# Kernel tuning notes

Measured on AMD Instinct MI355X. Metric: run time of the kernel, lower is better.

Reference implementation:

```python
import jax, jax.numpy as jnp
import numpy as np

N = 100000   # nodes
E = 1600000  # edges
D = 128      # in_channels (self and agg)
C = 128      # out_channels


def gcn_conv(x, W, b, src, dst, n):
    """PyG GCNConv: add self-loops, symmetric deg normalization, linear, scatter-add."""
    xw = x @ W  # [n, out]
    loops = jnp.arange(n)
    src2 = jnp.concatenate([src, loops])
    dst2 = jnp.concatenate([dst, loops])
    deg = jax.ops.segment_sum(jnp.ones_like(dst2, dtype=xw.dtype), dst2, num_segments=n)
    dinv = jnp.where(deg > 0, jax.lax.rsqrt(deg), 0.0)
    norm = dinv[src2] * dinv[dst2]  # [E+n]
    msg = xw[src2] * norm[:, None]  # gather + scale
    out = jax.ops.segment_sum(msg, dst2, num_segments=n)  # scatter-add at targets
    return out + b


def setup_inputs() -> dict:
    key = jax.random.key(0)
    ks = jax.random.split(key, 16)

    def w(k, shape):
        fan_in = shape[0]
        return (jax.random.uniform(k, shape, jnp.float32, -1.0, 1.0) / np.sqrt(fan_in)).astype(jnp.float32)

    inp = {
        "x_self": jax.random.normal(ks[0], (N, D), jnp.float32),
        "x_neighbor": jax.random.normal(ks[1], (N, D), jnp.float32),
        "edge_index": jax.random.randint(ks[2], (2, E), 0, N, dtype=jnp.int64),
        # linear_in_self: D -> 2C   (weights stored as [in, out])
        "W_in_self": w(ks[3], (D, 2 * C)),
        "b_in_self": w(ks[4], (2 * C,)),
        # linear_out_self: D + 2C -> C
        "W_out_self": w(ks[5], (D + 2 * C, C)),
        "b_out_self": w(ks[6], (C,)),
        # gcn1: D -> 2C ; gcn2: 2C -> C   (gcn3 unused in forward)
        "Wg1": w(ks[7], (D, 2 * C)),
        "bg1": w(ks[8], (2 * C,)),
        "Wg2": w(ks[9], (2 * C, C)),
        "bg2": w(ks[10], (C,)),
        # linear_out: D + 3C -> C
        "W_out": w(ks[11], (D + 3 * C, C)),
        "b_out": w(ks[12], (C,)),
    }
    return inp


def reference(x_self, x_neighbor, edge_index,
              W_in_self, b_in_self, W_out_self, b_out_self,
              Wg1, bg1, Wg2, bg2, W_out, b_out):
    src, dst = edge_index[0], edge_index[1]
    n = x_self.shape[0]

    # dense self branch
    l1 = jax.nn.relu(x_self @ W_in_self + b_in_self)          # [N, 2C]
    l1 = jnp.concatenate([x_self, l1], axis=1)                 # [N, D+2C]
    l1 = l1 @ W_out_self + b_out_self                          # [N, C]

    # GCN neighbor branch
    g1 = gcn_conv(x_neighbor, Wg1, bg1, src, dst, n)           # [N, 2C]
    g2 = gcn_conv(g1, Wg2, bg2, src, dst, n)                   # [N, C]
    x2 = jnp.concatenate([x_neighbor, g1, g2], axis=1)         # [N, D+3C]
    x2 = x2 @ W_out + b_out                                    # [N, C]

    return (l1, x2)
```

## Files before the change

### kernel.cpp

```cpp
#include <hip/hip_runtime.h>
#include <cstdint>
#include <cstddef>

#define NNODES 100000
#define NEDGES 1600000

typedef float f32x4 __attribute__((ext_vector_type(4)));
typedef unsigned int u32;
typedef _Float16 f16x2 __attribute__((ext_vector_type(2)));
typedef _Float16 f16x4 __attribute__((ext_vector_type(4)));
typedef _Float16 f16x8 __attribute__((ext_vector_type(8)));

__device__ __forceinline__ void gload_lds16(const void* g, void* l) {
  __builtin_amdgcn_global_load_lds((const __attribute__((address_space(1))) u32*)g,
                                   (__attribute__((address_space(3))) u32*)l, 16, 0, 0);
}


__global__ void zero_int_kernel(int* __restrict__ p, int n) {
  int i = blockIdx.x * blockDim.x + threadIdx.x;
  if (i < n) p[i] = 0;
}

__global__ void detect_kernel(const unsigned int* __restrict__ ei, int* __restrict__ flag) {
  unsigned int v = ei[2 * threadIdx.x + 1];
  unsigned long long b = __ballot(v != 0u);
  if (threadIdx.x == 0) *flag = (b == 0ull) ? 1 : 0;
}

__device__ __forceinline__ int edge_val(const void* ei, int is64, long long idx) {
  if (is64) return (int)((const long long*)ei)[idx];
  return ((const int*)ei)[idx];
}


__global__ void hist_kernel(const void* __restrict__ ei, const int* __restrict__ flag,
                            int* __restrict__ counts) {
  const int is64 = *flag;
  for (long long e = (long long)blockIdx.x * blockDim.x + threadIdx.x; e < NEDGES;
       e += (long long)gridDim.x * blockDim.x) {
    int d = edge_val(ei, is64, NEDGES + e);
    atomicAdd(&counts[d], 1);
  }
}

__global__ void dinv_kernel(const int* __restrict__ counts, float* __restrict__ dinv) {
  int i = blockIdx.x * blockDim.x + threadIdx.x;
  if (i < NNODES) dinv[i] = rsqrtf((float)(counts[i] + 1));
}

#define SCAN_B 256
#define SCAN_TILE 1024

__global__ void scan_reduce_kernel(const int* __restrict__ counts, int* __restrict__ bsums) {
  __shared__ int sd[SCAN_B];
  int t = threadIdx.x;
  int base = blockIdx.x * SCAN_TILE + t * 4;
  int s = 0;
#pragma unroll
  for (int i = 0; i < 4; i++) {
    int idx = base + i;
    if (idx < NNODES) s += counts[idx];
  }
  sd[t] = s;
  __syncthreads();
  for (int o = SCAN_B / 2; o > 0; o >>= 1) {
    if (t < o) sd[t] += sd[t + o];
    __syncthreads();
  }
  if (t == 0) bsums[blockIdx.x] = sd[0];
}

__global__ void scan_bsums_kernel(int* __restrict__ bsums, int* __restrict__ offs, int nb) {
  if (threadIdx.x == 0 && blockIdx.x == 0) {
    int run = 0;
    for (int b = 0; b < nb; b++) {
      int v = bsums[b];
      bsums[b] = run;
      run += v;
    }
    offs[NNODES] = run;
  }
}

__global__ void scan_write_kernel(const int* __restrict__ counts, const int* __restrict__ bsums,
                                  int* __restrict__ offs) {
  __shared__ int sd[SCAN_B];
  int t = threadIdx.x;
  int base = blockIdx.x * SCAN_TILE + t * 4;
  int v[4];
  int s = 0;
#pragma unroll
  for (int i = 0; i < 4; i++) {
    int idx = base + i;
    v[i] = (idx < NNODES) ? counts[idx] : 0;
    s += v[i];
  }
  sd[t] = s;
  __syncthreads();
  for (int o = 1; o < SCAN_B; o <<= 1) {
    int x = (t >= o) ? sd[t - o] : 0;
    __syncthreads();
    sd[t] += x;
    __syncthreads();
  }
  int run = sd[t] - s + bsums[blockIdx.x];
#pragma unroll
  for (int i = 0; i < 4; i++) {
    int idx = base + i;
    if (idx < NNODES) {
      offs[idx] = run;
      run += v[i];
    }
  }
}


#define BK_SHIFT 8
#define NBUCK 391
#define BCAP 8192
#define WCAP 12288

__global__ __launch_bounds__(256) void bucket_kernel(
    const void* __restrict__ ei, const int* __restrict__ flag, const int* __restrict__ offs,
    int* __restrict__ fillc, int* __restrict__ gcount,
    unsigned long long* __restrict__ bpairs, int* __restrict__ csr) {
  __shared__ int lcount[NBUCK];
  __shared__ int gbase[NBUCK];
  __shared__ int lcur[NBUCK];
  const int is64 = *flag;
  const int chunk = NEDGES / 256;
  const long long e0 = (long long)blockIdx.x * chunk;
  const long long e1 = e0 + chunk;
  for (int i = threadIdx.x; i < NBUCK; i += 256) {
    lcount[i] = 0;
    lcur[i] = 0;
  }
  __syncthreads();
  for (long long e = e0 + threadIdx.x; e < e1; e += 256) {
    int d = edge_val(ei, is64, NEDGES + e);
    atomicAdd(&lcount[d >> BK_SHIFT], 1);
  }
  __syncthreads();
  for (int i = threadIdx.x; i < NBUCK; i += 256) {
    int c = lcount[i];
    gbase[i] = c ? atomicAdd(&gcount[i], c) : 0;
  }
  __syncthreads();
  for (long long e = e0 + threadIdx.x; e < e1; e += 256) {
    int s = edge_val(ei, is64, e);
    int d = edge_val(ei, is64, NEDGES + e);
    int b = d >> BK_SHIFT;
    int pos = gbase[b] + atomicAdd(&lcur[b], 1);
    if (pos < BCAP) {
      bpairs[(size_t)b * BCAP + pos] =
          ((unsigned long long)(unsigned)d << 32) | (unsigned)s;
    } else {
      int p = offs[d] + atomicAdd(&fillc[d], 1);
      csr[p] = s;
    }
  }
}

__global__ __launch_bounds__(256) void fillwin_kernel(
    const unsigned long long* __restrict__ bpairs, const int* __restrict__ gcount,
    const int* __restrict__ offs, int* __restrict__ fillc, int* __restrict__ csr) {
  __shared__ int win[WCAP];
  __shared__ int nfill[256];
  const int b = blockIdx.x;
  const int nlo = b << BK_SHIFT;
  const int nhi = min(nlo + 256, NNODES);
  const int base = offs[nlo];
  const int W = offs[nhi] - base;
  int cnt = gcount[b];
  if (cnt > BCAP) cnt = BCAP;
  if (W <= WCAP) {
    if ((int)threadIdx.x < nhi - nlo) nfill[threadIdx.x] = fillc[nlo + threadIdx.x];
    for (int i = threadIdx.x; i < W; i += 256) win[i] = csr[base + i];
    __syncthreads();
    for (int i = threadIdx.x; i < cnt; i += 256) {
      unsigned long long v = bpairs[(size_t)b * BCAP + i];
      int d = (int)(v >> 32);
      int s = (int)(v & 0xffffffffull);
      int p = offs[d] - base + atomicAdd(&nfill[d - nlo], 1);
      win[p] = s;
    }
    __syncthreads();
    for (int i = threadIdx.x; i < W; i += 256) csr[base + i] = win[i];
  } else {
    for (int i = threadIdx.x; i < cnt; i += 256) {
      unsigned long long v = bpairs[(size_t)b * BCAP + i];
      int d = (int)(v >> 32);
      int s = (int)(v & 0xffffffffull);
      int p = offs[d] + atomicAdd(&fillc[d], 1);
      csr[p] = s;
    }
  }
}


__global__ void xcvt_kernel(const float* __restrict__ x, f16x4* __restrict__ y, int n4) {
  int i = blockIdx.x * blockDim.x + threadIdx.x;
  if (i >= n4) return;
  float4 v = ((const float4*)x)[i];
  f16x4 h;
  h[0] = (_Float16)v.x;
  h[1] = (_Float16)v.y;
  h[2] = (_Float16)v.z;
  h[3] = (_Float16)v.w;
  y[i] = h;
}


__global__ void prescale16_kernel(const f16x4* __restrict__ x, const float* __restrict__ dinv,
                                  f16x4* __restrict__ y) {
  int i = blockIdx.x * blockDim.x + threadIdx.x;
  if (i >= NNODES * 32) return;
  int row = i >> 5;
  float s = dinv[row];
  f16x4 v = x[i];
  f16x4 h;
  h[0] = (_Float16)((float)v[0] * s);
  h[1] = (_Float16)((float)v[1] * s);
  h[2] = (_Float16)((float)v[2] * s);
  h[3] = (_Float16)((float)v[3] * s);
  y[i] = h;
}


__device__ __forceinline__ float2 f16x2_to_f32(f16x2 h) {
  return make_float2((float)h[0], (float)h[1]);
}

__global__ __launch_bounds__(256) void aggregate_half_kernel(
    const f16x2* __restrict__ in, void* __restrict__ out, int out_half,
    const int* __restrict__ offs, const int* __restrict__ csr, const float* __restrict__ dinv,
    const float* __restrict__ bias) {
  int node = blockIdx.x * 4 + (threadIdx.x >> 6);
  if (node >= NNODES) return;
  int ch = threadIdx.x & 63;
  int beg = offs[node], end = offs[node + 1];

  float2 a0 = f16x2_to_f32(in[(size_t)node * 64 + ch]);
  float2 a1 = make_float2(0.f, 0.f);
  float2 a2 = make_float2(0.f, 0.f);
  float2 a3 = make_float2(0.f, 0.f);

  int p = beg;
  for (; p + 8 <= end; p += 8) {
    int j0 = csr[p + 0], j1 = csr[p + 1], j2 = csr[p + 2], j3 = csr[p + 3];
    int j4 = csr[p + 4], j5 = csr[p + 5], j6 = csr[p + 6], j7 = csr[p + 7];
    f16x2 h0 = in[(size_t)j0 * 64 + ch];
    f16x2 h1 = in[(size_t)j1 * 64 + ch];
    f16x2 h2 = in[(size_t)j2 * 64 + ch];
    f16x2 h3 = in[(size_t)j3 * 64 + ch];
    f16x2 h4 = in[(size_t)j4 * 64 + ch];
    f16x2 h5 = in[(size_t)j5 * 64 + ch];
    f16x2 h6 = in[(size_t)j6 * 64 + ch];
    f16x2 h7 = in[(size_t)j7 * 64 + ch];
    float2 v0 = f16x2_to_f32(h0);
    float2 v1 = f16x2_to_f32(h1);
    float2 v2 = f16x2_to_f32(h2);
    float2 v3 = f16x2_to_f32(h3);
    float2 v4 = f16x2_to_f32(h4);
    float2 v5 = f16x2_to_f32(h5);
    float2 v6 = f16x2_to_f32(h6);
    float2 v7 = f16x2_to_f32(h7);
    a0.x += v0.x; a0.y += v0.y;
    a1.x += v1.x; a1.y += v1.y;
    a2.x += v2.x; a2.y += v2.y;
    a3.x += v3.x; a3.y += v3.y;
    a0.x += v4.x; a0.y += v4.y;
    a1.x += v5.x; a1.y += v5.y;
    a2.x += v6.x; a2.y += v6.y;
    a3.x += v7.x; a3.y += v7.y;
  }
  for (; p + 2 <= end; p += 2) {
    int j0 = csr[p], j1 = csr[p + 1];
    float2 v0 = f16x2_to_f32(in[(size_t)j0 * 64 + ch]);
    float2 v1 = f16x2_to_f32(in[(size_t)j1 * 64 + ch]);
    a0.x += v0.x; a0.y += v0.y;
    a1.x += v1.x; a1.y += v1.y;
  }
  if (p < end) {
    float2 v0 = f16x2_to_f32(in[(size_t)csr[p] * 64 + ch]);
    a0.x += v0.x; a0.y += v0.y;
  }

  float di = dinv[node];
  int c = ch * 2;
  float2 r;
  r.x = di * (a0.x + a1.x + a2.x + a3.x);
  r.y = di * (a0.y + a1.y + a2.y + a3.y);
  if (bias) {
    r.x += bias[c];
    r.y += bias[c + 1];
  }
  if (out_half) {
    f16x2 h;
    h[0] = (_Float16)r.x;
    h[1] = (_Float16)r.y;
    ((f16x2*)out)[(size_t)node * 64 + ch] = h;
  } else {
    *(float2*)((float*)out + (size_t)node * 128 + c) = r;
  }
}


__global__ void wprep_f16_kernel(const float* __restrict__ W, int K, int M,
                                 _Float16* __restrict__ th) {
  int i = blockIdx.x * blockDim.x + threadIdx.x;
  if (i >= K * M) return;
  int k = i / M, m = i - k * M;
  th[(size_t)m * K + k] = (_Float16)W[i];
}


#define BM 128
#define BN 128
#define BK 32

__global__ __launch_bounds__(256) void gemm_f16_kernel(
    const _Float16* __restrict__ A0, int K0, const _Float16* __restrict__ A1, int K1,
    const _Float16* __restrict__ A2, int K2, const _Float16* __restrict__ Bth, int Ktot, int M,
    const float* __restrict__ bias, const float* __restrict__ row_scale,
    void* __restrict__ Cmat, int relu, int out_half, int nrows) {
  __shared__ _Float16 smem[4 * BM * BK];
  _Float16* const As0 = smem;
  _Float16* const Bs0 = smem + 2 * BM * BK;

  const int tid = threadIdx.x;
  const int lane = tid & 63;
  const int wv = tid >> 6;
  const int mBase = (wv >> 1) * 64;
  const int nBase = (wv & 1) * 64;
  const int ml = lane & 15;
  const int quad = lane >> 4;
  const int rowBase = blockIdx.x * BM;
  const int colBase = blockIdx.y * BN;

  const int lrow = lane >> 2;
  const int lslot = lane & 3;

  f32x4 acc[4][4];
  const f32x4 zero = {0.f, 0.f, 0.f, 0.f};
#pragma unroll
  for (int i = 0; i < 4; i++)
#pragma unroll
    for (int j = 0; j < 4; j++) acc[i][j] = zero;

  auto stage = [&](int k0, int buf) {
    const _Float16* Ap;
    int kl, Kp;
    if (k0 < K0) {
      Ap = A0; kl = k0; Kp = K0;
    } else if (k0 < K0 + K1) {
      Ap = A1; kl = k0 - K0; Kp = K1;
    } else {
      Ap = A2; kl = k0 - K0 - K1; Kp = K2;
    }
    char* Ab = (char*)(As0 + buf * BM * BK);
    char* Bb = (char*)(Bs0 + buf * BN * BK);
#pragma unroll
    for (int c = 0; c < 2; c++) {
      int trow = wv * 32 + c * 16 + lrow;
      int sws = lslot ^ (trow & 3);
      size_t ldsoff = (size_t)(wv * 32 + c * 16) * 64;
      int gr = rowBase + trow;
      if (gr > nrows - 1) gr = nrows - 1;
      gload_lds16(Ap + (size_t)gr * Kp + kl + sws * 8, Ab + ldsoff);
      gload_lds16(Bth + (size_t)(colBase + trow) * Ktot + k0 + sws * 8, Bb + ldsoff);
    }
  };

  const int ntile = Ktot / BK;
  stage(0, 0);
  __syncthreads();
  int cur = 0;
  for (int t = 0; t < ntile; ++t) {
    if (t + 1 < ntile) stage((t + 1) * BK, cur ^ 1);

    f16x8 av[4], bv[4];
#pragma unroll
    for (int nt = 0; nt < 4; nt++) {
      int nrow = nBase + nt * 16 + ml;
      int boff = nrow * 32 + ((quad ^ (nrow & 3)) << 3);
      bv[nt] = *(const f16x8*)&Bs0[cur * BN * BK + boff];
    }
#pragma unroll
    for (int mt = 0; mt < 4; mt++) {
      int mrow = mBase + mt * 16 + ml;
      int aoff = mrow * 32 + ((quad ^ (mrow & 3)) << 3);
      av[mt] = *(const f16x8*)&As0[cur * BM * BK + aoff];
    }
#pragma unroll
    for (int mt = 0; mt < 4; mt++)
#pragma unroll
      for (int nt = 0; nt < 4; nt++) {
        acc[mt][nt] =
            __builtin_amdgcn_mfma_f32_16x16x32_f16(av[mt], bv[nt], acc[mt][nt], 0, 0, 0);
      }
    __syncthreads();
    cur ^= 1;
  }

  if (out_half) {
    _Float16* Ct = smem;
#pragma unroll
    for (int nt = 0; nt < 4; nt++) {
      int colL = nBase + nt * 16 + ml;
      float bv = bias ? bias[colBase + colL] : 0.f;
#pragma unroll
      for (int mt = 0; mt < 4; mt++) {
        int rowL0 = mBase + mt * 16 + quad * 4;
#pragma unroll
        for (int r = 0; r < 4; r++) {
          int rowL = rowL0 + r;
          int grow = rowBase + rowL;
          float v = acc[mt][nt][r];
          if (row_scale) v *= row_scale[grow < nrows ? grow : nrows - 1];
          v += bv;
          if (relu) v = fmaxf(v, 0.f);
          Ct[rowL * 128 + colL] = (_Float16)v;
        }
      }
    }
    __syncthreads();
    for (int idx = tid; idx < 2048; idx += 256) {
      int rowL = idx >> 4;
      int chunk = idx & 15;
      int grow = rowBase + rowL;
      if (grow < nrows) {
        *(uint4*)((_Float16*)Cmat + (size_t)grow * M + colBase + chunk * 8) =
            *(const uint4*)&Ct[rowL * 128 + chunk * 8];
      }
    }
  } else {
#pragma unroll
    for (int nt = 0; nt < 4; nt++) {
      int col = colBase + nBase + nt * 16 + ml;
      float bv = bias ? bias[col] : 0.f;
#pragma unroll
      for (int mt = 0; mt < 4; mt++) {
        int row0 = rowBase + mBase + mt * 16 + quad * 4;
#pragma unroll
        for (int r = 0; r < 4; r++) {
          int grow = row0 + r;
          if (grow >= nrows) continue;
          float v = acc[mt][nt][r];
          if (row_scale) v *= row_scale[grow];
          v += bv;
          if (relu) v = fmaxf(v, 0.f);
          ((float*)Cmat)[(size_t)grow * M + col] = v;
        }
      }
    }
  }
}


extern "C" void kernel_launch(void* const* d_in, const int* in_sizes, int n_in, void* d_out,
                              int out_size, void* d_ws, size_t ws_size, hipStream_t stream) {
  const float* x_self     = (const float*)d_in[0];
  const float* x_neighbor = (const float*)d_in[1];
  const void*  edge_index = d_in[2];
  const float* W_in_self  = (const float*)d_in[3];
  const float* b_in_self  = (const float*)d_in[4];
  const float* W_out_self = (const float*)d_in[5];
  const float* b_out_self = (const float*)d_in[6];
  const float* Wg1        = (const float*)d_in[7];
  const float* bg1        = (const float*)d_in[8];
  const float* Wg2        = (const float*)d_in[9];
  const float* bg2        = (const float*)d_in[10];
  const float* W_out      = (const float*)d_in[11];
  const float* b_out      = (const float*)d_in[12];
  float* out = (float*)d_out;

  char* ws = (char*)d_ws;
  size_t off = 0;
  auto alloc = [&](size_t bytes) -> void* {
    void* p = ws + off;
    off = (off + bytes + 255) & ~(size_t)255;
    return p;
  };
  int* counts = (int*)alloc((size_t)2 * NNODES * 4 + 2048);
  int* fillc  = counts + NNODES;
  int* gcount = counts + 2 * NNODES;
  int*   offs   = (int*)alloc((size_t)(NNODES + 1) * 4);
  int*   csr    = (int*)alloc((size_t)NEDGES * 4);
  int*   bsums  = (int*)alloc(4096);
  int*   flag   = (int*)alloc(256);
  float* dinv   = (float*)alloc((size_t)NNODES * 4);
  _Float16* wt1 = (_Float16*)alloc(32768 * 2);
  _Float16* wt2 = (_Float16*)alloc(49152 * 2);
  _Float16* wt3 = (_Float16*)alloc(32768 * 2);
  _Float16* wt4 = (_Float16*)alloc(32768 * 2);
  _Float16* wt5 = (_Float16*)alloc(65536 * 2);
  float* bufA = (float*)alloc((size_t)NNODES * 256 * 4);
  float* bufB = (float*)alloc((size_t)NNODES * 256 * 4);
  (void)ws_size;

  unsigned long long* bpairs = (unsigned long long*)bufA;

  const int nb = (NNODES + SCAN_TILE - 1) / SCAN_TILE;
  const int gridRows = (NNODES + BM - 1) / BM;

  detect_kernel<<<1, 64, 0, stream>>>((const unsigned int*)edge_index, flag);
  zero_int_kernel<<<(2 * NNODES + 512 + 255) / 256, 256, 0, stream>>>(counts,
                                                                      2 * NNODES + 512);
  hist_kernel<<<1024, 256, 0, stream>>>(edge_index, flag, counts);
  dinv_kernel<<<(NNODES + 255) / 256, 256, 0, stream>>>(counts, dinv);
  scan_reduce_kernel<<<nb, SCAN_B, 0, stream>>>(counts, bsums);
  scan_bsums_kernel<<<1, 64, 0, stream>>>(bsums, offs, nb);
  scan_write_kernel<<<nb, SCAN_B, 0, stream>>>(counts, bsums, offs);
  bucket_kernel<<<256, 256, 0, stream>>>(edge_index, flag, offs, fillc, gcount, bpairs, csr);
  fillwin_kernel<<<NBUCK, 256, 0, stream>>>(bpairs, gcount, offs, fillc, csr);

  wprep_f16_kernel<<<(32768 + 255) / 256, 256, 0, stream>>>(W_in_self, 128, 256, wt1);
  wprep_f16_kernel<<<(49152 + 255) / 256, 256, 0, stream>>>(W_out_self, 384, 128, wt2);
  wprep_f16_kernel<<<(32768 + 255) / 256, 256, 0, stream>>>(Wg1, 128, 256, wt3);
  wprep_f16_kernel<<<(32768 + 255) / 256, 256, 0, stream>>>(Wg2, 256, 128, wt4);
  wprep_f16_kernel<<<(65536 + 255) / 256, 256, 0, stream>>>(W_out, 512, 128, wt5);

  _Float16* xs16 = (_Float16*)(bufB + (size_t)NNODES * 128);
  _Float16* xn16 = xs16 + (size_t)NNODES * 128;
  xcvt_kernel<<<(NNODES * 32 + 255) / 256, 256, 0, stream>>>(x_self, (f16x4*)xs16, NNODES * 32);
  xcvt_kernel<<<(NNODES * 32 + 255) / 256, 256, 0, stream>>>(x_neighbor, (f16x4*)xn16,
                                                             NNODES * 32);

  _Float16* l1 = (_Float16*)bufA;
  gemm_f16_kernel<<<dim3(gridRows, 2), 256, 0, stream>>>(
      xs16, 128, nullptr, 0, nullptr, 0, wt1, 128, 256, b_in_self, nullptr, l1, 1, 1, NNODES);
  gemm_f16_kernel<<<dim3(gridRows, 1), 256, 0, stream>>>(
      xs16, 128, l1, 256, nullptr, 0, wt2, 384, 128, b_out_self, nullptr, out, 0, 0, NNODES);

  _Float16* ybuf = (_Float16*)bufB;
  _Float16* aggx = (_Float16*)bufA;
  _Float16* g1   = (_Float16*)bufB;
  _Float16* xw2  = (_Float16*)bufA;
  _Float16* g2   = (_Float16*)bufA + (size_t)NNODES * 128;

  prescale16_kernel<<<(NNODES * 32 + 255) / 256, 256, 0, stream>>>((const f16x4*)xn16, dinv,
                                                                   (f16x4*)ybuf);
  aggregate_half_kernel<<<NNODES / 4, 256, 0, stream>>>((const f16x2*)ybuf, aggx, 1, offs, csr,
                                                        dinv, nullptr);
  gemm_f16_kernel<<<dim3(gridRows, 2), 256, 0, stream>>>(
      aggx, 128, nullptr, 0, nullptr, 0, wt3, 128, 256, bg1, nullptr, g1, 0, 1, NNODES);
  gemm_f16_kernel<<<dim3(gridRows, 1), 256, 0, stream>>>(
      g1, 256, nullptr, 0, nullptr, 0, wt4, 256, 128, nullptr, dinv, xw2, 0, 1, NNODES);
  aggregate_half_kernel<<<NNODES / 4, 256, 0, stream>>>((const f16x2*)xw2, g2, 1, offs, csr,
                                                        dinv, bg2);
  gemm_f16_kernel<<<dim3(gridRows, 1), 256, 0, stream>>>(
      xn16, 128, g1, 256, g2, 128, wt5, 512, 128, b_out, nullptr,
      out + (size_t)NNODES * 128, 0, 0, NNODES);
}
```

Before: 674.4 us.

## Fuse degree histogram into bucket pass and fuse fp16 convert with prescale

The bucketing pass now runs before the prefix scan and also counts destination degrees, so the separate histogram pass over the edge list goes away. Edges that overflow a bucket are written to a side list and scattered into the CSR by a new small kernel once offsets exist. Separately, x_neighbor is converted to fp16 and prescaled by dinv in a single kernel, which removes the prescale pass that reread the fp16 copy. The cost is extra global atomics on counts inside the bucket kernel, plus one contended atomic counter for the overflow list.

```diff
diff --git a/kernel.cpp b/kernel.cpp
--- a/kernel.cpp
+++ b/kernel.cpp
@@ -33,16 +33,6 @@
   return ((const int*)ei)[idx];
 }
 
-
-__global__ void hist_kernel(const void* __restrict__ ei, const int* __restrict__ flag,
-                            int* __restrict__ counts) {
-  const int is64 = *flag;
-  for (long long e = (long long)blockIdx.x * blockDim.x + threadIdx.x; e < NEDGES;
-       e += (long long)gridDim.x * blockDim.x) {
-    int d = edge_val(ei, is64, NEDGES + e);
-    atomicAdd(&counts[d], 1);
-  }
-}
 
 __global__ void dinv_kernel(const int* __restrict__ counts, float* __restrict__ dinv) {
   int i = blockIdx.x * blockDim.x + threadIdx.x;
@@ -122,9 +112,9 @@
 #define WCAP 12288
 
 __global__ __launch_bounds__(256) void bucket_kernel(
-    const void* __restrict__ ei, const int* __restrict__ flag, const int* __restrict__ offs,
-    int* __restrict__ fillc, int* __restrict__ gcount,
-    unsigned long long* __restrict__ bpairs, int* __restrict__ csr) {
+    const void* __restrict__ ei, const int* __restrict__ flag, int* __restrict__ counts,
+    int* __restrict__ gcount, unsigned long long* __restrict__ bpairs,
+    unsigned long long* __restrict__ ovf, int* __restrict__ novf) {
   __shared__ int lcount[NBUCK];
   __shared__ int gbase[NBUCK];
   __shared__ int lcur[NBUCK];
@@ -140,6 +130,7 @@
   for (long long e = e0 + threadIdx.x; e < e1; e += 256) {
     int d = edge_val(ei, is64, NEDGES + e);
     atomicAdd(&lcount[d >> BK_SHIFT], 1);
+    atomicAdd(&counts[d], 1);
   }
   __syncthreads();
   for (int i = threadIdx.x; i < NBUCK; i += 256) {
@@ -152,13 +143,27 @@
     int d = edge_val(ei, is64, NEDGES + e);
     int b = d >> BK_SHIFT;
     int pos = gbase[b] + atomicAdd(&lcur[b], 1);
+    unsigned long long pair = ((unsigned long long)(unsigned)d << 32) | (unsigned)s;
     if (pos < BCAP) {
-      bpairs[(size_t)b * BCAP + pos] =
-          ((unsigned long long)(unsigned)d << 32) | (unsigned)s;
+      bpairs[(size_t)b * BCAP + pos] = pair;
     } else {
-      int p = offs[d] + atomicAdd(&fillc[d], 1);
-      csr[p] = s;
-    }
+      int o = atomicAdd(novf, 1);
+      ovf[o] = pair;
+    }
+  }
+}
+
+__global__ void ovf_scatter_kernel(const unsigned long long* __restrict__ ovf,
+                                   const int* __restrict__ novf, const int* __restrict__ offs,
+                                   int* __restrict__ fillc, int* __restrict__ csr) {
+  int n = *novf;
+  for (int i = blockIdx.x * blockDim.x + threadIdx.x; i < n;
+       i += gridDim.x * blockDim.x) {
+    unsigned long long v = ovf[i];
+    int d = (int)(v >> 32);
+    int s = (int)(v & 0xffffffffull);
+    int p = offs[d] + atomicAdd(&fillc[d], 1);
+    csr[p] = s;
   }
 }
 
@@ -211,20 +216,24 @@
   y[i] = h;
 }
 
-
-__global__ void prescale16_kernel(const f16x4* __restrict__ x, const float* __restrict__ dinv,
-                                  f16x4* __restrict__ y) {
+__global__ void xcvt2_kernel(const float* __restrict__ x, const float* __restrict__ dinv,
+                             f16x4* __restrict__ xn, f16x4* __restrict__ yb) {
   int i = blockIdx.x * blockDim.x + threadIdx.x;
   if (i >= NNODES * 32) return;
   int row = i >> 5;
   float s = dinv[row];
-  f16x4 v = x[i];
-  f16x4 h;
-  h[0] = (_Float16)((float)v[0] * s);
-  h[1] = (_Float16)((float)v[1] * s);
-  h[2] = (_Float16)((float)v[2] * s);
-  h[3] = (_Float16)((float)v[3] * s);
-  y[i] = h;
+  float4 v = ((const float4*)x)[i];
+  f16x4 h, hp;
+  h[0] = (_Float16)v.x;
+  h[1] = (_Float16)v.y;
+  h[2] = (_Float16)v.z;
+  h[3] = (_Float16)v.w;
+  hp[0] = (_Float16)(v.x * s);
+  hp[1] = (_Float16)(v.y * s);
+  hp[2] = (_Float16)(v.z * s);
+  hp[3] = (_Float16)(v.w * s);
+  xn[i] = h;
+  yb[i] = hp;
 }
 
 
@@ -486,6 +495,7 @@
   int* counts = (int*)alloc((size_t)2 * NNODES * 4 + 2048);
   int* fillc  = counts + NNODES;
   int* gcount = counts + 2 * NNODES;
+  int* novf   = gcount + NBUCK;
   int*   offs   = (int*)alloc((size_t)(NNODES + 1) * 4);
   int*   csr    = (int*)alloc((size_t)NEDGES * 4);
   int*   bsums  = (int*)alloc(4096);
@@ -501,6 +511,7 @@
   (void)ws_size;
 
   unsigned long long* bpairs = (unsigned long long*)bufA;
+  unsigned long long* ovf = (unsigned long long*)bufB;
 
   const int nb = (NNODES + SCAN_TILE - 1) / SCAN_TILE;
   const int gridRows = (NNODES + BM - 1) / BM;
@@ -508,12 +519,12 @@
   detect_kernel<<<1, 64, 0, stream>>>((const unsigned int*)edge_index, flag);
   zero_int_kernel<<<(2 * NNODES + 512 + 255) / 256, 256, 0, stream>>>(counts,
                                                                       2 * NNODES + 512);
-  hist_kernel<<<1024, 256, 0, stream>>>(edge_index, flag, counts);
+  bucket_kernel<<<256, 256, 0, stream>>>(edge_index, flag, counts, gcount, bpairs, ovf, novf);
   dinv_kernel<<<(NNODES + 255) / 256, 256, 0, stream>>>(counts, dinv);
   scan_reduce_kernel<<<nb, SCAN_B, 0, stream>>>(counts, bsums);
   scan_bsums_kernel<<<1, 64, 0, stream>>>(bsums, offs, nb);
   scan_write_kernel<<<nb, SCAN_B, 0, stream>>>(counts, bsums, offs);
-  bucket_kernel<<<256, 256, 0, stream>>>(edge_index, flag, offs, fillc, gcount, bpairs, csr);
+  ovf_scatter_kernel<<<64, 256, 0, stream>>>(ovf, novf, offs, fillc, csr);
   fillwin_kernel<<<NBUCK, 256, 0, stream>>>(bpairs, gcount, offs, fillc, csr);
 
   wprep_f16_kernel<<<(32768 + 255) / 256, 256, 0, stream>>>(W_in_self, 128, 256, wt1);
@@ -524,9 +535,10 @@
 
   _Float16* xs16 = (_Float16*)(bufB + (size_t)NNODES * 128);
   _Float16* xn16 = xs16 + (size_t)NNODES * 128;
+  _Float16* ybuf = (_Float16*)bufB;
   xcvt_kernel<<<(NNODES * 32 + 255) / 256, 256, 0, stream>>>(x_self, (f16x4*)xs16, NNODES * 32);
-  xcvt_kernel<<<(NNODES * 32 + 255) / 256, 256, 0, stream>>>(x_neighbor, (f16x4*)xn16,
-                                                             NNODES * 32);
+  xcvt2_kernel<<<(NNODES * 32 + 255) / 256, 256, 0, stream>>>(x_neighbor, dinv, (f16x4*)xn16,
+                                                              (f16x4*)ybuf);
 
   _Float16* l1 = (_Float16*)bufA;
   gemm_f16_kernel<<<dim3(gridRows, 2), 256, 0, stream>>>(
@@ -534,14 +546,11 @@
   gemm_f16_kernel<<<dim3(gridRows, 1), 256, 0, stream>>>(
       xs16, 128, l1, 256, nullptr, 0, wt2, 384, 128, b_out_self, nullptr, out, 0, 0, NNODES);
 
-  _Float16* ybuf = (_Float16*)bufB;
   _Float16* aggx = (_Float16*)bufA;
   _Float16* g1   = (_Float16*)bufB;
   _Float16* xw2  = (_Float16*)bufA;
   _Float16* g2   = (_Float16*)bufA + (size_t)NNODES * 128;
 
-  prescale16_kernel<<<(NNODES * 32 + 255) / 256, 256, 0, stream>>>((const f16x4*)xn16, dinv,
-                                                                   (f16x4*)ybuf);
   aggregate_half_kernel<<<NNODES / 4, 256, 0, stream>>>((const f16x2*)ybuf, aggx, 1, offs, csr,
                                                         dinv, nullptr);
   gemm_f16_kernel<<<dim3(gridRows, 2), 256, 0, stream>>>(
```

After: 660.3 us. 1.02x faster.
